# Kernel tuning notes

Hardware: AMD Instinct MI355X
Metric: run time of the kernel (lower is better)

## Reference

```python
import jax, jax.numpy as jnp
import numpy as np

B, T, C = 32, 4000, 128
FLOOR = 1e-12


def setup_inputs() -> dict:
    key = jax.random.key(0)
    k1, = jax.random.split(key, 1)
    x = jax.random.uniform(k1, (B, T, C), dtype=jnp.float32)  # non-negative energies
    # learned params (init values per module defaults)
    alpha = jnp.full((C,), 0.96, dtype=jnp.float32)
    delta = jnp.full((C,), 2.0, dtype=jnp.float32)
    root = jnp.full((C,), 2.0, dtype=jnp.float32)
    ema_weights = jnp.full((C,), 0.04, dtype=jnp.float32)  # per-channel smooth coef (sPCEN)
    return {"x": x, "alpha": alpha, "delta": delta, "root": root, "ema_weights": ema_weights}


def _ema(x, w):
    # x: (B,T,C), w: (C,) clamped to [0,1]; acc_t = w*x_t + (1-w)*acc_{t-1}, acc_{-1} = x_0
    w = jnp.clip(w, 0.0, 1.0).astype(x.dtype)
    init = x[:, 0, :]  # (B,C)

    def step(acc, xt):
        acc = w * xt + (1.0 - w) * acc
        return acc, acc

    _, ys = jax.lax.scan(step, init, jnp.swapaxes(x, 0, 1))  # ys: (T,B,C)
    return jnp.swapaxes(ys, 0, 1)  # (B,T,C)


def reference(x, alpha, delta, root, ema_weights):
    alpha = jnp.minimum(alpha, 1.0).astype(x.dtype)  # (C,)
    root = jnp.maximum(root, 1.0).astype(x.dtype)
    delta = delta.astype(x.dtype)
    ema = _ema(x, ema_weights)  # (B,T,C)
    one_over_root = 1.0 / root
    out = (x / (FLOOR + ema) ** alpha + delta) ** one_over_root - delta ** one_over_root
    return out
```

## Files before the change

### kernel.cpp

```cpp
#include <hip/hip_runtime.h>


#define FLOOR_EPS 1e-12f

constexpr int Bn = 32;
constexpr int Tn = 4000;
constexpr int Cn = 128;
constexpr int NCHUNK = 125;
constexpr int CHUNK  = 32;

__global__ __launch_bounds__(Cn) void k1_localsum(
    const float* __restrict__ x,
    const float* __restrict__ w_p,
    float* __restrict__ out)
{
    __shared__ float tile[CHUNK * Cn];
    const int tid = threadIdx.x;
    const int j = blockIdx.x;
    const int b = blockIdx.y;
    const size_t base = ((size_t)b * Tn + (size_t)j * CHUNK) * (size_t)Cn;

    const float4* __restrict__ g4 = (const float4*)(x + base);
    float4* t4 = (float4*)tile;
    #pragma unroll
    for (int k = 0; k < 8; ++k)
        t4[k * Cn + tid] = g4[k * Cn + tid];
    __syncthreads();

    const int c = tid;
    const float w   = fminf(fmaxf(w_p[c], 0.0f), 1.0f);
    const float omw = 1.0f - w;
    float s = 0.0f;
    #pragma unroll
    for (int k = 0; k < CHUNK; ++k)
        s = fmaf(omw, s, w * tile[k * Cn + c]);
    out[base + Cn + c] = s;
}

__global__ __launch_bounds__(256) void k2_scan(
    const float* __restrict__ x,
    const float* __restrict__ w_p,
    float* __restrict__ out)
{
    const int wid  = (blockIdx.x * 256 + threadIdx.x) >> 6;
    const int lane = threadIdx.x & 63;
    const int b = wid >> 7;
    const int c = wid & 127;

    const float w   = fminf(fmaxf(w_p[c], 0.0f), 1.0f);
    const float omw = 1.0f - w;
    const float A = __builtin_exp2f((float)CHUNK * __builtin_log2f(omw));

    const float* __restrict__ sb = out + (size_t)b * Tn * Cn + c;
    float* __restrict__ eb       = out + (size_t)b * Tn * Cn + c;

    float s1 = sb[((size_t)lane * CHUNK + 1) * Cn];
    float a1 = A;
    const int j2 = 64 + lane;
    float s2 = (j2 < NCHUNK) ? sb[((size_t)j2 * CHUNK + 1) * Cn] : 0.0f;
    float a2 = (j2 < NCHUNK) ? A : 1.0f;

    #pragma unroll
    for (int r = 1; r < 64; r <<= 1) {
        float ts = __shfl_up(s1, r, 64);
        float ta = __shfl_up(a1, r, 64);
        if (lane >= r) { s1 = fmaf(a1, ts, s1); a1 *= ta; }
        ts = __shfl_up(s2, r, 64);
        ta = __shfl_up(a2, r, 64);
        if (lane >= r) { s2 = fmaf(a2, ts, s2); a2 *= ta; }
    }

    const float e0 = x[(size_t)b * Tn * Cn + c];
    const float E1 = fmaf(a1, e0, s1);
    const float E64 = __shfl(E1, 63, 64);
    const float E2 = fmaf(a2, E64, s2);

    if (lane == 0) eb[0] = e0;
    eb[(size_t)(lane + 1) * CHUNK * Cn] = E1;
    if (lane + 65 < NCHUNK)
        eb[(size_t)(lane + 65) * CHUNK * Cn] = E2;
}

__global__ __launch_bounds__(Cn) void k3_apply(
    const float* __restrict__ x,
    const float* __restrict__ alpha_p,
    const float* __restrict__ delta_p,
    const float* __restrict__ root_p,
    const float* __restrict__ w_p,
    float* __restrict__ out)
{
    __shared__ float tile[CHUNK * Cn];
    const int tid = threadIdx.x;
    const int j = blockIdx.x;
    const int b = blockIdx.y;
    const size_t base = ((size_t)b * Tn + (size_t)j * CHUNK) * (size_t)Cn;

    const float4* __restrict__ g4 = (const float4*)(x + base);
    float4* t4 = (float4*)tile;
    #pragma unroll
    for (int k = 0; k < 8; ++k)
        t4[k * Cn + tid] = g4[k * Cn + tid];

    const int c = tid;
    const float alpha  = fminf(alpha_p[c], 1.0f);
    const float root   = fmaxf(root_p[c], 1.0f);
    const float delta  = delta_p[c];
    const float oor    = 1.0f / root;
    const float droot  = __builtin_exp2f(oor * __builtin_log2f(delta));
    const float nalpha = -alpha;
    const float w      = fminf(fmaxf(w_p[c], 0.0f), 1.0f);
    const float omw    = 1.0f - w;

    const float E = out[base + c];
    __syncthreads();

    float acc = E;
    #pragma unroll
    for (int k = 0; k < CHUNK; ++k) {
        const float xv = tile[k * Cn + c];
        acc = fmaf(omw, acc, w * xv);
        const float l  = __builtin_log2f(FLOOR_EPS + acc);
        const float t1 = xv * __builtin_exp2f(nalpha * l);
        tile[k * Cn + c] =
            __builtin_exp2f(oor * __builtin_log2f(t1 + delta)) - droot;
    }
    __syncthreads();

    float4* o4 = (float4*)(out + base);
    #pragma unroll
    for (int k = 0; k < 8; ++k)
        o4[k * Cn + tid] = t4[k * Cn + tid];
}

extern "C" void kernel_launch(void* const* d_in, const int* in_sizes, int n_in,
                              void* d_out, int out_size, void* d_ws, size_t ws_size,
                              hipStream_t stream) {
    const float* x     = (const float*)d_in[0];
    const float* alpha = (const float*)d_in[1];
    const float* delta = (const float*)d_in[2];
    const float* root  = (const float*)d_in[3];
    const float* ew    = (const float*)d_in[4];
    float* out = (float*)d_out;

    dim3 grid(NCHUNK, Bn, 1);
    k1_localsum<<<grid, Cn, 0, stream>>>(x, ew, out);
    k2_scan<<<dim3((Bn * Cn * 64) / 256), 256, 0, stream>>>(x, ew, out);
    k3_apply<<<grid, Cn, 0, stream>>>(x, alpha, delta, root, ew, out);
}
```

Before: 133.7 us.

## Fuse chunk-carry scan into apply kernel using workspace chunk sums

Replaces the three-kernel local-sum/scan/apply pipeline with two kernels when a workspace is available. Chunk local sums go to a compact workspace buffer, and each apply block computes its own carry-in by serially folding all preceding chunk sums. This removes one launch and the separate scan pass. In exchange, later chunks do up to 124 sequential dependent FMAs with strided loads, and total redundant carry work grows quadratically in the number of chunks.

Result: slower. 145.3 us (+8.6%).

```diff
diff --git a/kernel.cpp b/kernel.cpp
--- a/kernel.cpp
+++ b/kernel.cpp
@@ -8,6 +8,92 @@
 constexpr int Cn = 128;
 constexpr int NCHUNK = 125;
 constexpr int CHUNK  = 32;
+
+__global__ __launch_bounds__(Cn) void d1_localsum(
+    const float* __restrict__ x,
+    const float* __restrict__ w_p,
+    float* __restrict__ S)
+{
+    __shared__ float tile[CHUNK * Cn];
+    const int tid = threadIdx.x;
+    const int j = blockIdx.x;
+    const int b = blockIdx.y;
+    const size_t base = ((size_t)b * Tn + (size_t)j * CHUNK) * (size_t)Cn;
+
+    const float4* __restrict__ g4 = (const float4*)(x + base);
+    float4* t4 = (float4*)tile;
+    #pragma unroll
+    for (int k = 0; k < 8; ++k)
+        t4[k * Cn + tid] = g4[k * Cn + tid];
+    __syncthreads();
+
+    const int c = tid;
+    const float w   = fminf(fmaxf(w_p[c], 0.0f), 1.0f);
+    const float omw = 1.0f - w;
+    float s = 0.0f;
+    #pragma unroll
+    for (int k = 0; k < CHUNK; ++k)
+        s = fmaf(omw, s, w * tile[k * Cn + c]);
+    S[((size_t)b * NCHUNK + j) * Cn + c] = s;
+}
+
+__global__ __launch_bounds__(Cn) void d2_apply(
+    const float* __restrict__ x,
+    const float* __restrict__ alpha_p,
+    const float* __restrict__ delta_p,
+    const float* __restrict__ root_p,
+    const float* __restrict__ w_p,
+    const float* __restrict__ S,
+    float* __restrict__ out)
+{
+    __shared__ float tile[CHUNK * Cn];
+    const int tid = threadIdx.x;
+    const int j = blockIdx.x;
+    const int b = blockIdx.y;
+    const size_t base = ((size_t)b * Tn + (size_t)j * CHUNK) * (size_t)Cn;
+
+    const float4* __restrict__ g4 = (const float4*)(x + base);
+    float4* t4 = (float4*)tile;
+    #pragma unroll
+    for (int k = 0; k < 8; ++k)
+        t4[k * Cn + tid] = g4[k * Cn + tid];
+
+    const int c = tid;
+    const float w   = fminf(fmaxf(w_p[c], 0.0f), 1.0f);
+    const float omw = 1.0f - w;
+    const float A = __builtin_exp2f((float)CHUNK * __builtin_log2f(omw));
+
+    float e = x[(size_t)b * Tn * Cn + c];
+    const float* __restrict__ sp = S + (size_t)b * NCHUNK * Cn + c;
+    #pragma unroll 4
+    for (int i = 0; i < j; ++i)
+        e = fmaf(A, e, sp[(size_t)i * Cn]);
+
+    const float alpha  = fminf(alpha_p[c], 1.0f);
+    const float root   = fmaxf(root_p[c], 1.0f);
+    const float delta  = delta_p[c];
+    const float oor    = 1.0f / root;
+    const float droot  = __builtin_exp2f(oor * __builtin_log2f(delta));
+    const float nalpha = -alpha;
+    __syncthreads();
+
+    float acc = e;
+    #pragma unroll
+    for (int k = 0; k < CHUNK; ++k) {
+        const float xv = tile[k * Cn + c];
+        acc = fmaf(omw, acc, w * xv);
+        const float l  = __builtin_log2f(FLOOR_EPS + acc);
+        const float t1 = xv * __builtin_exp2f(nalpha * l);
+        tile[k * Cn + c] =
+            __builtin_exp2f(oor * __builtin_log2f(t1 + delta)) - droot;
+    }
+    __syncthreads();
+
+    float4* o4 = (float4*)(out + base);
+    #pragma unroll
+    for (int k = 0; k < 8; ++k)
+        o4[k * Cn + tid] = t4[k * Cn + tid];
+}
 
 __global__ __launch_bounds__(Cn) void k1_localsum(
     const float* __restrict__ x,
@@ -142,8 +228,16 @@
     const float* ew    = (const float*)d_in[4];
     float* out = (float*)d_out;
 
+    const size_t ws_needed = (size_t)Bn * NCHUNK * Cn * sizeof(float);
     dim3 grid(NCHUNK, Bn, 1);
-    k1_localsum<<<grid, Cn, 0, stream>>>(x, ew, out);
-    k2_scan<<<dim3((Bn * Cn * 64) / 256), 256, 0, stream>>>(x, ew, out);
-    k3_apply<<<grid, Cn, 0, stream>>>(x, alpha, delta, root, ew, out);
-}
+
+    if (d_ws != nullptr && ws_size >= ws_needed) {
+        float* S = (float*)d_ws;
+        d1_localsum<<<grid, Cn, 0, stream>>>(x, ew, S);
+        d2_apply<<<grid, Cn, 0, stream>>>(x, alpha, delta, root, ew, S, out);
+    } else {
+        k1_localsum<<<grid, Cn, 0, stream>>>(x, ew, out);
+        k2_scan<<<dim3((Bn * Cn * 64) / 256), 256, 0, stream>>>(x, ew, out);
+        k3_apply<<<grid, Cn, 0, stream>>>(x, alpha, delta, root, ew, out);
+    }
+}
```

## Fuse EMA scan and PCEN into one striped kernel with truncated warm-up

Applied to the files above, without the earlier changes.

Replaces the three-kernel chunked scan (local sums, cross-chunk prefix scan, apply) with a single kernel. The time axis is split into 16 stripes per batch, and each stripe rebuilds its starting EMA state by replaying up to 256 earlier steps from zero, relying on the decay (1-w)^256 being negligible. If the decay is not small enough, it falls back to replaying from t=0, which stays exact. This removes two launches and the intermediate round trips through the output buffer. In exchange it adds redundant warm-up reads, accepts a small truncation error, and leaves only 512 blocks, each running a long serial, latency-bound chain per thread.

New measurement: 169.5 us. 26.7% more time.

```diff
diff --git a/kernel.cpp b/kernel.cpp
--- a/kernel.cpp
+++ b/kernel.cpp
@@ -6,82 +6,11 @@
 constexpr int Bn = 32;
 constexpr int Tn = 4000;
 constexpr int Cn = 128;
-constexpr int NCHUNK = 125;
-constexpr int CHUNK  = 32;
+constexpr int NS      = 16;
+constexpr int LSTRIPE = Tn / NS;
+constexpr int HWARM   = 256;
 
-__global__ __launch_bounds__(Cn) void k1_localsum(
-    const float* __restrict__ x,
-    const float* __restrict__ w_p,
-    float* __restrict__ out)
-{
-    __shared__ float tile[CHUNK * Cn];
-    const int tid = threadIdx.x;
-    const int j = blockIdx.x;
-    const int b = blockIdx.y;
-    const size_t base = ((size_t)b * Tn + (size_t)j * CHUNK) * (size_t)Cn;
-
-    const float4* __restrict__ g4 = (const float4*)(x + base);
-    float4* t4 = (float4*)tile;
-    #pragma unroll
-    for (int k = 0; k < 8; ++k)
-        t4[k * Cn + tid] = g4[k * Cn + tid];
-    __syncthreads();
-
-    const int c = tid;
-    const float w   = fminf(fmaxf(w_p[c], 0.0f), 1.0f);
-    const float omw = 1.0f - w;
-    float s = 0.0f;
-    #pragma unroll
-    for (int k = 0; k < CHUNK; ++k)
-        s = fmaf(omw, s, w * tile[k * Cn + c]);
-    out[base + Cn + c] = s;
-}
-
-__global__ __launch_bounds__(256) void k2_scan(
-    const float* __restrict__ x,
-    const float* __restrict__ w_p,
-    float* __restrict__ out)
-{
-    const int wid  = (blockIdx.x * 256 + threadIdx.x) >> 6;
-    const int lane = threadIdx.x & 63;
-    const int b = wid >> 7;
-    const int c = wid & 127;
-
-    const float w   = fminf(fmaxf(w_p[c], 0.0f), 1.0f);
-    const float omw = 1.0f - w;
-    const float A = __builtin_exp2f((float)CHUNK * __builtin_log2f(omw));
-
-    const float* __restrict__ sb = out + (size_t)b * Tn * Cn + c;
-    float* __restrict__ eb       = out + (size_t)b * Tn * Cn + c;
-
-    float s1 = sb[((size_t)lane * CHUNK + 1) * Cn];
-    float a1 = A;
-    const int j2 = 64 + lane;
-    float s2 = (j2 < NCHUNK) ? sb[((size_t)j2 * CHUNK + 1) * Cn] : 0.0f;
-    float a2 = (j2 < NCHUNK) ? A : 1.0f;
-
-    #pragma unroll
-    for (int r = 1; r < 64; r <<= 1) {
-        float ts = __shfl_up(s1, r, 64);
-        float ta = __shfl_up(a1, r, 64);
-        if (lane >= r) { s1 = fmaf(a1, ts, s1); a1 *= ta; }
-        ts = __shfl_up(s2, r, 64);
-        ta = __shfl_up(a2, r, 64);
-        if (lane >= r) { s2 = fmaf(a2, ts, s2); a2 *= ta; }
-    }
-
-    const float e0 = x[(size_t)b * Tn * Cn + c];
-    const float E1 = fmaf(a1, e0, s1);
-    const float E64 = __shfl(E1, 63, 64);
-    const float E2 = fmaf(a2, E64, s2);
-
-    if (lane == 0) eb[0] = e0;
-    eb[(size_t)(lane + 1) * CHUNK * Cn] = E1;
-    if (lane + 65 < NCHUNK)
-        eb[(size_t)(lane + 65) * CHUNK * Cn] = E2;
-}
-
-__global__ __launch_bounds__(Cn) void k3_apply(
+__global__ __launch_bounds__(Cn) void pcen_stripe(
     const float* __restrict__ x,
     const float* __restrict__ alpha_p,
     const float* __restrict__ delta_p,
@@ -89,47 +18,71 @@
     const float* __restrict__ w_p,
     float* __restrict__ out)
 {
-    __shared__ float tile[CHUNK * Cn];
-    const int tid = threadIdx.x;
-    const int j = blockIdx.x;
-    const int b = blockIdx.y;
-    const size_t base = ((size_t)b * Tn + (size_t)j * CHUNK) * (size_t)Cn;
+    const int c  = threadIdx.x;
+    const int s  = blockIdx.x;
+    const int b  = blockIdx.y;
+    const int t0 = s * LSTRIPE;
+    const int t1 = t0 + LSTRIPE;
 
-    const float4* __restrict__ g4 = (const float4*)(x + base);
-    float4* t4 = (float4*)tile;
-    #pragma unroll
-    for (int k = 0; k < 8; ++k)
-        t4[k * Cn + tid] = g4[k * Cn + tid];
-
-    const int c = tid;
+    const float w   = fminf(fmaxf(w_p[c], 0.0f), 1.0f);
+    const float omw = 1.0f - w;
     const float alpha  = fminf(alpha_p[c], 1.0f);
     const float root   = fmaxf(root_p[c], 1.0f);
     const float delta  = delta_p[c];
     const float oor    = 1.0f / root;
     const float droot  = __builtin_exp2f(oor * __builtin_log2f(delta));
     const float nalpha = -alpha;
-    const float w      = fminf(fmaxf(w_p[c], 0.0f), 1.0f);
-    const float omw    = 1.0f - w;
 
-    const float E = out[base + c];
-    __syncthreads();
+    const float* __restrict__ xb = x   + (size_t)b * Tn * Cn + c;
+    float* __restrict__       ob = out + (size_t)b * Tn * Cn + c;
 
-    float acc = E;
-    #pragma unroll
-    for (int k = 0; k < CHUNK; ++k) {
-        const float xv = tile[k * Cn + c];
-        acc = fmaf(omw, acc, w * xv);
-        const float l  = __builtin_log2f(FLOOR_EPS + acc);
-        const float t1 = xv * __builtin_exp2f(nalpha * l);
-        tile[k * Cn + c] =
-            __builtin_exp2f(oor * __builtin_log2f(t1 + delta)) - droot;
+    int   ts;
+    float e;
+    if (t0 == 0) {
+        ts = 0; e = xb[0];
+    } else {
+        const int   W = (t0 < HWARM) ? t0 : HWARM;
+        const float decay = __builtin_exp2f((float)W * __builtin_log2f(omw));
+        if (decay > 3e-3f) { ts = 0;      e = xb[0]; }
+        else               { ts = t0 - W; e = 0.0f;  }
     }
-    __syncthreads();
 
-    float4* o4 = (float4*)(out + base);
-    #pragma unroll
-    for (int k = 0; k < 8; ++k)
-        o4[k * Cn + tid] = t4[k * Cn + tid];
+    const float* xq = xb + (size_t)ts * Cn;
+    int t = ts;
+    for (; t + 16 <= t0; t += 16) {
+        float v[16];
+        #pragma unroll
+        for (int k = 0; k < 16; ++k) v[k] = xq[(size_t)k * Cn];
+        #pragma unroll
+        for (int k = 0; k < 16; ++k) e = fmaf(omw, e, w * v[k]);
+        xq += (size_t)16 * Cn;
+    }
+    for (; t < t0; ++t) { e = fmaf(omw, e, w * xq[0]); xq += Cn; }
+
+    float* oq = ob + (size_t)t0 * Cn;
+    for (t = t0; t + 4 <= t1; t += 4) {
+        float v[4];
+        #pragma unroll
+        for (int k = 0; k < 4; ++k) v[k] = xq[(size_t)k * Cn];
+        #pragma unroll
+        for (int k = 0; k < 4; ++k) {
+            e = fmaf(omw, e, w * v[k]);
+            const float l  = __builtin_log2f(FLOOR_EPS + e);
+            const float tv = v[k] * __builtin_exp2f(nalpha * l);
+            oq[(size_t)k * Cn] =
+                __builtin_exp2f(oor * __builtin_log2f(tv + delta)) - droot;
+        }
+        xq += (size_t)4 * Cn;
+        oq += (size_t)4 * Cn;
+    }
+    for (; t < t1; ++t) {
+        const float xv = xq[0];
+        e = fmaf(omw, e, w * xv);
+        const float l  = __builtin_log2f(FLOOR_EPS + e);
+        const float tv = xv * __builtin_exp2f(nalpha * l);
+        oq[0] = __builtin_exp2f(oor * __builtin_log2f(tv + delta)) - droot;
+        xq += Cn; oq += Cn;
+    }
 }
 
 extern "C" void kernel_launch(void* const* d_in, const int* in_sizes, int n_in,
@@ -142,8 +95,5 @@
     const float* ew    = (const float*)d_in[4];
     float* out = (float*)d_out;
 
-    dim3 grid(NCHUNK, Bn, 1);
-    k1_localsum<<<grid, Cn, 0, stream>>>(x, ew, out);
-    k2_scan<<<dim3((Bn * Cn * 64) / 256), 256, 0, stream>>>(x, ew, out);
-    k3_apply<<<grid, Cn, 0, stream>>>(x, alpha, delta, root, ew, out);
+    pcen_stripe<<<dim3(NS, Bn), Cn, 0, stream>>>(x, alpha, delta, root, ew, out);
 }
```
